# Kernel tuning notes

Hardware: AMD Instinct MI355X
Metric: run time of the kernel (lower is better)

## Reference

```python
import jax, jax.numpy as jnp
import numpy as np


def setup_inputs() -> dict:
    key = jax.random.key(0)
    ks = jax.random.split(key, 6)
    B, C1, C2, C, H, W = 16, 512, 320, 256, 64, 64
    x1 = jax.random.normal(ks[0], (B, C1, H, W), dtype=jnp.float32)
    x2 = jax.random.normal(ks[1], (B, C2, H, W), dtype=jnp.float32)
    # 1x1 conv weights, bias=False -> plain channel matmuls
    w_img = jax.random.normal(ks[2], (C, C1), dtype=jnp.float32) * (1.0 / np.sqrt(C1))
    w_txt = jax.random.normal(ks[3], (C, C2), dtype=jnp.float32) * (1.0 / np.sqrt(C2))
    w_out = jax.random.normal(ks[4], (C1, C), dtype=jnp.float32) * (1.0 / np.sqrt(C))
    gamma = jax.random.normal(ks[5], (1,), dtype=jnp.float32)
    return {"x1": x1, "x2": x2, "w_img": w_img, "w_txt": w_txt,
            "w_out": w_out, "gamma": gamma}


def reference(x1, x2, w_img, w_txt, w_out, gamma):
    B, _, H, W = x1.shape
    # 1x1 conv projections (bias-free) == channel matmuls
    img = jnp.einsum('oc,bchw->bohw', w_img, x1)   # [B,C,H,W]
    txt = jnp.einsum('oc,bchw->bohw', w_txt, x2)   # [B,C,H,W]
    C = img.shape[1]
    q = img.reshape(B, C, H * W)                    # [B,C,N]
    kv = txt.reshape(B, C, H * W)                   # [B,C,N]
    attn = jnp.einsum('bcn,bdn->bcd', q, kv)        # QK^T over spatial dim
    attn = jax.nn.softmax(attn, axis=-1)            # [B,C,C]
    attn_info = jnp.einsum('bcd,bdn->bcn', attn, kv).reshape(B, C, H, W)
    out = gamma[0] * attn_info + img                # scale-residual
    out = jnp.einsum('oc,bchw->bohw', w_out, out)   # output 1x1 conv
    return out
```

## Files before the change

### kernel.cpp

```cpp
#include <hip/hip_runtime.h>
#include <stdint.h>

typedef _Float16 f16_t;
typedef _Float16 f16x4 __attribute__((ext_vector_type(4)));
typedef _Float16 f16x8 __attribute__((ext_vector_type(8)));
typedef float f32x4 __attribute__((ext_vector_type(4)));

__device__ __forceinline__ void async16(const void* g, void* lds) {
    typedef __attribute__((address_space(3))) void lds_void;
    typedef __attribute__((address_space(1))) void glb_void;
    lds_void* l = (lds_void*)(unsigned int)(unsigned long long)lds;
    glb_void* gp = (glb_void*)(unsigned long long)g;
    __builtin_amdgcn_global_load_lds(gp, l, 16, 0, 0);
}

__global__ void cvt3_zero(const float* __restrict__ a, f16_t* __restrict__ oa, int na,
                          const float* __restrict__ b, f16_t* __restrict__ ob, int nb,
                          const float* __restrict__ c, f16_t* __restrict__ oc, int nc,
                          float4* __restrict__ z, int nz4) {
    int i = blockIdx.x * 256 + threadIdx.x;
    if (i < na) oa[i] = (f16_t)a[i];
    if (i < nb) ob[i] = (f16_t)b[i];
    if (i < nc) oc[i] = (f16_t)c[i];
    if (i < nz4) { float4 zz; zz.x = 0.f; zz.y = 0.f; zz.z = 0.f; zz.w = 0.f; z[i] = zz; }
}

template <typename TIN>
__global__ void transpose_cvt(const TIN* __restrict__ in, f16_t* __restrict__ out,
                              int R, int S, long long inStride, long long outStride) {
    __shared__ float tile[32][33];
    const int b = blockIdx.z;
    const TIN* ip = in + (long long)b * inStride;
    f16_t* op = out + (long long)b * outStride;
    const int s0 = blockIdx.x * 32;
    const int r0 = blockIdx.y * 32;
    const int t = threadIdx.x;
    const int lr = t >> 3;
    const int lc = (t & 7) * 4;

    const TIN* src = ip + (long long)(r0 + lr) * S + s0 + lc;
    float v0, v1, v2, v3;
    if (sizeof(TIN) == 4) {
        float4 v = *(const float4*)src;
        v0 = v.x; v1 = v.y; v2 = v.z; v3 = v.w;
    } else {
        f16x4 v = *(const f16x4*)src;
        v0 = (float)v[0]; v1 = (float)v[1]; v2 = (float)v[2]; v3 = (float)v[3];
    }
    tile[lr][lc + 0] = v0;
    tile[lr][lc + 1] = v1;
    tile[lr][lc + 2] = v2;
    tile[lr][lc + 3] = v3;
    __syncthreads();

    const int sr = t >> 3;
    const int rc = (t & 7) * 4;
    f16x4 o;
    o[0] = (f16_t)tile[rc + 0][sr];
    o[1] = (f16_t)tile[rc + 1][sr];
    o[2] = (f16_t)tile[rc + 2][sr];
    o[3] = (f16_t)tile[rc + 3][sr];
    *(f16x4*)(op + (long long)(s0 + sr) * R + r0 + rc) = o;
}

template <int BM, int BN, int TM, int TN, int WM, int WN, int MODE, int KSPLIT>
__global__ __launch_bounds__(256, 2)
void gemm_bt(const f16_t* __restrict__ A, const f16_t* __restrict__ B,
             void* __restrict__ C, const f16_t* __restrict__ resid,
             const float* __restrict__ gamma, f16_t* __restrict__ Ct,
             int M, int N, int K,
             long long strideA, long long strideB, long long strideC,
             long long strideCt) {
    constexpr int BK = 32;
    __shared__ __align__(16) f16_t As[BM * BK];
    __shared__ __align__(16) f16_t Bs[BN * BK];
    __shared__ __align__(16) f16_t Lt[(MODE == 3) ? BN * (BM + 8) : 1];

    const int tid = threadIdx.x;
    const int wave = tid >> 6;
    const int lane = tid & 63;
    const int wm = wave / WN;
    const int wn = wave % WN;
    const int l16 = lane & 15;
    const int l4 = lane >> 4;

    const long long zb = (KSPLIT == 1) ? blockIdx.z : (blockIdx.z / KSPLIT);
    const int ks = (KSPLIT == 1) ? 0 : (blockIdx.z % KSPLIT);
    const int Ksl = K / KSPLIT;
    const f16_t* Ab = A + zb * strideA + (long long)blockIdx.y * BM * K;
    const f16_t* Bb = B + zb * strideB + (long long)blockIdx.x * BN * K;

    f32x4 zero = {0.f, 0.f, 0.f, 0.f};
    f32x4 acc[TM][TN];
#pragma unroll
    for (int i = 0; i < TM; ++i)
#pragma unroll
        for (int j = 0; j < TN; ++j) acc[i][j] = zero;

    const int kBeg = ks * Ksl;
    for (int k0 = kBeg; k0 < kBeg + Ksl; k0 += BK) {
#pragma unroll
        for (int r = 0; r < (BM * 4) / 256; ++r) {
            int seg = r * 256 + tid;
            const f16_t* g = Ab + (long long)(seg >> 2) * K + k0 + (seg & 3) * 8;
            async16(g, &As[(r * 256 + wave * 64) * 8]);
        }
#pragma unroll
        for (int r = 0; r < (BN * 4) / 256; ++r) {
            int seg = r * 256 + tid;
            const f16_t* g = Bb + (long long)(seg >> 2) * K + k0 + (seg & 3) * 8;
            async16(g, &Bs[(r * 256 + wave * 64) * 8]);
        }
        __syncthreads();

        f16x8 af[TM], bfr[TN];
#pragma unroll
        for (int i = 0; i < TM; ++i)
            af[i] = *(const f16x8*)&As[((wm * TM + i) * 16 + l16) * BK + l4 * 8];
#pragma unroll
        for (int j = 0; j < TN; ++j)
            bfr[j] = *(const f16x8*)&Bs[((wn * TN + j) * 16 + l16) * BK + l4 * 8];
#pragma unroll
        for (int i = 0; i < TM; ++i)
#pragma unroll
            for (int j = 0; j < TN; ++j)
                acc[i][j] = __builtin_amdgcn_mfma_f32_16x16x32_f16(af[i], bfr[j], acc[i][j], 0, 0, 0);
        __syncthreads();
    }

    const int row0 = blockIdx.y * BM + wm * TM * 16;
    const int col0 = blockIdx.x * BN + wn * TN * 16;
    float g = (MODE == 2) ? gamma[0] : 0.f;
#pragma unroll
    for (int i = 0; i < TM; ++i) {
#pragma unroll
        for (int j = 0; j < TN; ++j) {
            f16x4 tq;
#pragma unroll
            for (int r = 0; r < 4; ++r) {
                int row = row0 + i * 16 + l4 * 4 + r;
                int col = col0 + j * 16 + l16;
                long long idx = zb * strideC + (long long)row * N + col;
                float v = acc[i][j][r];
                if (MODE == 0) {
                    ((f16_t*)C)[idx] = (f16_t)v;
                } else if (MODE == 1) {
                    ((float*)C)[idx] = v;
                } else if (MODE == 2) {
                    float im = (float)resid[idx];
                    ((f16_t*)C)[idx] = (f16_t)(g * v + im);
                } else if (MODE == 3) {
                    ((f16_t*)C)[idx] = (f16_t)v;
                    tq[r] = (f16_t)v;
                } else if (MODE == 5) {
                    atomicAdd(&((float*)C)[idx], v);
                }
            }
            if (MODE == 3) {
                int rl = wm * (TM * 16) + i * 16 + l4 * 4;
                int cl = wn * (TN * 16) + j * 16 + l16;
                *(f16x4*)&Lt[cl * (BM + 8) + rl] = tq;
            }
        }
    }

    if (MODE == 3) {
        __syncthreads();
        const int bx0 = blockIdx.x * BN;
        const int by0 = blockIdx.y * BM;
        const long long cb = zb * strideCt;
#pragma unroll
        for (int it = 0; it < (BM * BN) / 2048; ++it) {
            int nl = it * 16 + (tid >> 4);
            int c8 = (tid & 15) * 8;
            f16x8 v = *(const f16x8*)&Lt[nl * (BM + 8) + c8];
            *(f16x8*)&Ct[cb + (long long)(bx0 + nl) * M + by0 + c8] = v;
        }
    }
}

__global__ void softmax256(const float* __restrict__ attn, f16_t* __restrict__ out) {
    const int row = blockIdx.x * 4 + (threadIdx.x >> 6);
    const int lane = threadIdx.x & 63;
    const float4 v = *(const float4*)(attn + (long long)row * 256 + lane * 4);
    float m = fmaxf(fmaxf(v.x, v.y), fmaxf(v.z, v.w));
#pragma unroll
    for (int off = 32; off > 0; off >>= 1) m = fmaxf(m, __shfl_xor(m, off, 64));
    float e0 = __expf(v.x - m), e1 = __expf(v.y - m);
    float e2 = __expf(v.z - m), e3 = __expf(v.w - m);
    float s = e0 + e1 + e2 + e3;
#pragma unroll
    for (int off = 32; off > 0; off >>= 1) s += __shfl_xor(s, off, 64);
    const float inv = 1.0f / s;
    f16x4 o;
    o[0] = (f16_t)(e0 * inv);
    o[1] = (f16_t)(e1 * inv);
    o[2] = (f16_t)(e2 * inv);
    o[3] = (f16_t)(e3 * inv);
    *(f16x4*)(out + (long long)row * 256 + lane * 4) = o;
}

extern "C" void kernel_launch(void* const* d_in, const int* in_sizes, int n_in,
                              void* d_out, int out_size, void* d_ws, size_t ws_size,
                              hipStream_t stream) {
    (void)in_sizes; (void)n_in; (void)out_size; (void)ws_size;

    const float* x1 = (const float*)d_in[0];
    const float* x2 = (const float*)d_in[1];
    const float* w_img = (const float*)d_in[2];
    const float* w_txt = (const float*)d_in[3];
    const float* w_out = (const float*)d_in[4];
    const float* gamma = (const float*)d_in[5];

    constexpr int B = 16, C1 = 512, C2 = 320, C = 256, N = 4096, OC = 512;
    constexpr long long NC = (long long)N * C;
    constexpr long long CC = (long long)C * C;

    char* ws = (char*)d_ws;
    f16_t* wib  = (f16_t*)(ws + 0);
    f16_t* wtb  = (f16_t*)(ws + 262144);
    f16_t* wob  = (f16_t*)(ws + 425984);
    f16_t* img  = (f16_t*)(ws + 688128);
    f16_t* imgT = (f16_t*)(ws + 34242560);
    f16_t* kvT  = (f16_t*)(ws + 67796992);
    f16_t* yT   = img;

    char* oc = (char*)d_out;
    f16_t* x1t   = (f16_t*)(oc);
    f16_t* x2t   = (f16_t*)(oc + 67108864);
    f16_t* kv    = (f16_t*)(oc);
    float* attn  = (float*)(oc + 109051904);
    f16_t* attns = (f16_t*)(oc + 113246208);

    cvt3_zero<<<1024, 256, 0, stream>>>(w_img, wib, C * C1,
                                        w_txt, wtb, C * C2,
                                        w_out, wob, OC * C,
                                        (float4*)attn, (int)(B * CC / 4));

    transpose_cvt<float><<<dim3(N / 32, C1 / 32, B), 256, 0, stream>>>(
        x1, x1t, C1, N, (long long)C1 * N, (long long)N * C1);
    transpose_cvt<float><<<dim3(N / 32, C2 / 32, B), 256, 0, stream>>>(
        x2, x2t, C2, N, (long long)C2 * N, (long long)N * C2);

    gemm_bt<128, 128, 4, 4, 2, 2, 3, 1><<<dim3(N / 128, C / 128, B), 256, 0, stream>>>(
        wib, x1t, img, nullptr, nullptr, imgT, C, N, C1,
        0LL, (long long)N * C1, NC, NC);

    gemm_bt<128, 128, 4, 4, 2, 2, 3, 1><<<dim3(C / 128, N / 128, B), 256, 0, stream>>>(
        x2t, wtb, kvT, nullptr, nullptr, kv, N, C, C2,
        (long long)N * C2, 0LL, NC, NC);

    gemm_bt<64, 64, 2, 2, 2, 2, 5, 4><<<dim3(C / 64, C / 64, B * 4), 256, 0, stream>>>(
        img, kv, attn, nullptr, nullptr, nullptr, C, C, N,
        NC, NC, CC, 0LL);

    softmax256<<<(B * C) / 4, 256, 0, stream>>>(attn, attns);

    gemm_bt<128, 128, 4, 4, 2, 2, 2, 1><<<dim3(C / 128, N / 128, B), 256, 0, stream>>>(
        kvT, attns, yT, imgT, gamma, nullptr, N, C, C,
        NC, CC, NC, 0LL);

    gemm_bt<128, 128, 4, 4, 2, 2, 1, 1><<<dim3(N / 128, OC / 128, B), 256, 0, stream>>>(
        wob, yT, (float*)d_out, nullptr, nullptr, nullptr, OC, N, C,
        0LL, NC, (long long)OC * N, 0LL);
}
```

Before: 473.6 us.

## Double-buffer GEMM loads, merge prep kernels, replace atomic split-K with partial-sum reduction

After: 452.5 us. 1.05x faster.

```diff
diff --git a/kernel.cpp b/kernel.cpp
--- a/kernel.cpp
+++ b/kernel.cpp
@@ -14,53 +14,49 @@
     __builtin_amdgcn_global_load_lds(gp, l, 16, 0, 0);
 }
 
-__global__ void cvt3_zero(const float* __restrict__ a, f16_t* __restrict__ oa, int na,
-                          const float* __restrict__ b, f16_t* __restrict__ ob, int nb,
-                          const float* __restrict__ c, f16_t* __restrict__ oc, int nc,
-                          float4* __restrict__ z, int nz4) {
-    int i = blockIdx.x * 256 + threadIdx.x;
-    if (i < na) oa[i] = (f16_t)a[i];
-    if (i < nb) ob[i] = (f16_t)b[i];
-    if (i < nc) oc[i] = (f16_t)c[i];
-    if (i < nz4) { float4 zz; zz.x = 0.f; zz.y = 0.f; zz.z = 0.f; zz.w = 0.f; z[i] = zz; }
-}
-
-template <typename TIN>
-__global__ void transpose_cvt(const TIN* __restrict__ in, f16_t* __restrict__ out,
-                              int R, int S, long long inStride, long long outStride) {
+__global__ __launch_bounds__(256) void prep(
+    const float* __restrict__ x1, const float* __restrict__ x2,
+    f16_t* __restrict__ x1t, f16_t* __restrict__ x2t,
+    const float* __restrict__ w_img, f16_t* __restrict__ wib,
+    const float* __restrict__ w_txt, f16_t* __restrict__ wtb,
+    const float* __restrict__ w_out, f16_t* __restrict__ wob) {
     __shared__ float tile[32][33];
-    const int b = blockIdx.z;
-    const TIN* ip = in + (long long)b * inStride;
-    f16_t* op = out + (long long)b * outStride;
-    const int s0 = blockIdx.x * 32;
-    const int r0 = blockIdx.y * 32;
+    const int id = blockIdx.x;
     const int t = threadIdx.x;
-    const int lr = t >> 3;
-    const int lc = (t & 7) * 4;
-
-    const TIN* src = ip + (long long)(r0 + lr) * S + s0 + lc;
-    float v0, v1, v2, v3;
-    if (sizeof(TIN) == 4) {
-        float4 v = *(const float4*)src;
-        v0 = v.x; v1 = v.y; v2 = v.z; v3 = v.w;
+    if (id < 53248) {
+        const float* ip; f16_t* op; int R, bx, by, bz;
+        const int S = 4096;
+        if (id < 32768) {
+            R = 512; bx = id & 127; by = (id >> 7) & 15; bz = id >> 11;
+            ip = x1 + (long long)bz * R * S;
+            op = x1t + (long long)bz * S * R;
+        } else {
+            const int id2 = id - 32768;
+            R = 320; bx = id2 & 127; by = (id2 >> 7) % 10; bz = id2 / 1280;
+            ip = x2 + (long long)bz * R * S;
+            op = x2t + (long long)bz * S * R;
+        }
+        const int s0 = bx * 32, r0 = by * 32;
+        const int lr = t >> 3, lc = (t & 7) * 4;
+        const float4 v = *(const float4*)(ip + (long long)(r0 + lr) * S + s0 + lc);
+        tile[lr][lc + 0] = v.x;
+        tile[lr][lc + 1] = v.y;
+        tile[lr][lc + 2] = v.z;
+        tile[lr][lc + 3] = v.w;
+        __syncthreads();
+        const int sr = t >> 3, rc = (t & 7) * 4;
+        f16x4 o;
+        o[0] = (f16_t)tile[rc + 0][sr];
+        o[1] = (f16_t)tile[rc + 1][sr];
+        o[2] = (f16_t)tile[rc + 2][sr];
+        o[3] = (f16_t)tile[rc + 3][sr];
+        *(f16x4*)(op + (long long)(s0 + sr) * R + r0 + rc) = o;
     } else {
-        f16x4 v = *(const f16x4*)src;
-        v0 = (float)v[0]; v1 = (float)v[1]; v2 = (float)v[2]; v3 = (float)v[3];
-    }
-    tile[lr][lc + 0] = v0;
-    tile[lr][lc + 1] = v1;
-    tile[lr][lc + 2] = v2;
-    tile[lr][lc + 3] = v3;
-    __syncthreads();
-
-    const int sr = t >> 3;
-    const int rc = (t & 7) * 4;
-    f16x4 o;
-    o[0] = (f16_t)tile[rc + 0][sr];
-    o[1] = (f16_t)tile[rc + 1][sr];
-    o[2] = (f16_t)tile[rc + 2][sr];
-    o[3] = (f16_t)tile[rc + 3][sr];
-    *(f16x4*)(op + (long long)(s0 + sr) * R + r0 + rc) = o;
+        const int i = (id - 53248) * 256 + t;
+        if (i < 512 * 256) wib[i] = (f16_t)w_img[i];
+        if (i < 320 * 256) wtb[i] = (f16_t)w_txt[i];
+        if (i < 512 * 256) wob[i] = (f16_t)w_out[i];
+    }
 }
 
 template <int BM, int BN, int TM, int TN, int WM, int WN, int MODE, int KSPLIT>
@@ -72,9 +68,12 @@
              long long strideA, long long strideB, long long strideC,
              long long strideCt) {
     constexpr int BK = 32;
-    __shared__ __align__(16) f16_t As[BM * BK];
-    __shared__ __align__(16) f16_t Bs[BN * BK];
-    __shared__ __align__(16) f16_t Lt[(MODE == 3) ? BN * (BM + 8) : 1];
+    constexpr int AS = BM * BK;
+    constexpr int BS = BN * BK;
+    constexpr int STG = AS + BS;
+    constexpr int LT = (MODE == 3) ? BN * (BM + 8) : 0;
+    constexpr int POOL = (2 * STG > LT) ? 2 * STG : LT;
+    __shared__ __align__(16) f16_t pool[POOL];
 
     const int tid = threadIdx.x;
     const int wave = tid >> 6;
@@ -97,8 +96,9 @@
 #pragma unroll
         for (int j = 0; j < TN; ++j) acc[i][j] = zero;
 
-    const int kBeg = ks * Ksl;
-    for (int k0 = kBeg; k0 < kBeg + Ksl; k0 += BK) {
+    auto stage = [&](int b, int k0) {
+        f16_t* As = pool + b * STG;
+        f16_t* Bs = As + AS;
 #pragma unroll
         for (int r = 0; r < (BM * 4) / 256; ++r) {
             int seg = r * 256 + tid;
@@ -111,8 +111,10 @@
             const f16_t* g = Bb + (long long)(seg >> 2) * K + k0 + (seg & 3) * 8;
             async16(g, &Bs[(r * 256 + wave * 64) * 8]);
         }
-        __syncthreads();
-
+    };
+    auto compute = [&](int b) {
+        const f16_t* As = pool + b * STG;
+        const f16_t* Bs = As + AS;
         f16x8 af[TM], bfr[TN];
 #pragma unroll
         for (int i = 0; i < TM; ++i)
@@ -125,8 +127,22 @@
 #pragma unroll
             for (int j = 0; j < TN; ++j)
                 acc[i][j] = __builtin_amdgcn_mfma_f32_16x16x32_f16(af[i], bfr[j], acc[i][j], 0, 0, 0);
+    };
+
+    const int kBeg = ks * Ksl;
+    const int NT = Ksl / BK;
+    stage(0, kBeg);
+    __syncthreads();
+    int cur = 0;
+    for (int t = 1; t < NT; ++t) {
+        stage(cur ^ 1, kBeg + t * BK);
+        compute(cur);
         __syncthreads();
-    }
+        cur ^= 1;
+    }
+    compute(cur);
+
+    if (MODE == 3) __syncthreads();
 
     const int row0 = blockIdx.y * BM + wm * TM * 16;
     const int col0 = blockIdx.x * BN + wn * TN * 16;
@@ -140,26 +156,29 @@
             for (int r = 0; r < 4; ++r) {
                 int row = row0 + i * 16 + l4 * 4 + r;
                 int col = col0 + j * 16 + l16;
-                long long idx = zb * strideC + (long long)row * N + col;
                 float v = acc[i][j][r];
-                if (MODE == 0) {
-                    ((f16_t*)C)[idx] = (f16_t)v;
-                } else if (MODE == 1) {
+                if (MODE == 4) {
+                    long long idx = (long long)blockIdx.z * strideC + (long long)row * N + col;
                     ((float*)C)[idx] = v;
-                } else if (MODE == 2) {
-                    float im = (float)resid[idx];
-                    ((f16_t*)C)[idx] = (f16_t)(g * v + im);
-                } else if (MODE == 3) {
-                    ((f16_t*)C)[idx] = (f16_t)v;
-                    tq[r] = (f16_t)v;
-                } else if (MODE == 5) {
-                    atomicAdd(&((float*)C)[idx], v);
+                } else {
+                    long long idx = zb * strideC + (long long)row * N + col;
+                    if (MODE == 0) {
+                        ((f16_t*)C)[idx] = (f16_t)v;
+                    } else if (MODE == 1) {
+                        ((float*)C)[idx] = v;
+                    } else if (MODE == 2) {
+                        float im = (float)resid[idx];
+                        ((f16_t*)C)[idx] = (f16_t)(g * v + im);
+                    } else if (MODE == 3) {
+                        ((f16_t*)C)[idx] = (f16_t)v;
+                        tq[r] = (f16_t)v;
+                    }
                 }
             }
             if (MODE == 3) {
                 int rl = wm * (TM * 16) + i * 16 + l4 * 4;
                 int cl = wn * (TN * 16) + j * 16 + l16;
-                *(f16x4*)&Lt[cl * (BM + 8) + rl] = tq;
+                *(f16x4*)&pool[cl * (BM + 8) + rl] = tq;
             }
         }
     }
@@ -169,20 +188,30 @@
         const int bx0 = blockIdx.x * BN;
         const int by0 = blockIdx.y * BM;
         const long long cb = zb * strideCt;
-#pragma unroll
-        for (int it = 0; it < (BM * BN) / 2048; ++it) {
-            int nl = it * 16 + (tid >> 4);
-            int c8 = (tid & 15) * 8;
-            f16x8 v = *(const f16x8*)&Lt[nl * (BM + 8) + c8];
+        constexpr int TPR = BM / 8;
+        constexpr int RPI = 256 / TPR;
+#pragma unroll
+        for (int it = 0; it < BN / RPI; ++it) {
+            int nl = it * RPI + (tid / TPR);
+            int c8 = (tid % TPR) * 8;
+            f16x8 v = *(const f16x8*)&pool[nl * (BM + 8) + c8];
             *(f16x8*)&Ct[cb + (long long)(bx0 + nl) * M + by0 + c8] = v;
         }
     }
 }
 
-__global__ void softmax256(const float* __restrict__ attn, f16_t* __restrict__ out) {
+template <int KS>
+__global__ void softmax_red(const float* __restrict__ part, f16_t* __restrict__ out) {
     const int row = blockIdx.x * 4 + (threadIdx.x >> 6);
     const int lane = threadIdx.x & 63;
-    const float4 v = *(const float4*)(attn + (long long)row * 256 + lane * 4);
+    const int b = row >> 8, r = row & 255;
+    const float* p = part + (long long)(b * KS) * 65536 + r * 256 + lane * 4;
+    float4 v = *(const float4*)p;
+#pragma unroll
+    for (int k = 1; k < KS; ++k) {
+        float4 u = *(const float4*)(p + (long long)k * 65536);
+        v.x += u.x; v.y += u.y; v.z += u.z; v.w += u.w;
+    }
     float m = fmaxf(fmaxf(v.x, v.y), fmaxf(v.z, v.w));
 #pragma unroll
     for (int off = 32; off > 0; off >>= 1) m = fmaxf(m, __shfl_xor(m, off, 64));
@@ -197,7 +226,7 @@
     o[1] = (f16_t)(e1 * inv);
     o[2] = (f16_t)(e2 * inv);
     o[3] = (f16_t)(e3 * inv);
-    *(f16x4*)(out + (long long)row * 256 + lane * 4) = o;
+    *(f16x4*)(out + ((long long)row) * 256 + lane * 4) = o;
 }
 
 extern "C" void kernel_launch(void* const* d_in, const int* in_sizes, int n_in,
@@ -213,54 +242,47 @@
     const float* gamma = (const float*)d_in[5];
 
     constexpr int B = 16, C1 = 512, C2 = 320, C = 256, N = 4096, OC = 512;
+    constexpr int KS = 8;
     constexpr long long NC = (long long)N * C;
     constexpr long long CC = (long long)C * C;
 
     char* ws = (char*)d_ws;
-    f16_t* wib  = (f16_t*)(ws + 0);
-    f16_t* wtb  = (f16_t*)(ws + 262144);
-    f16_t* wob  = (f16_t*)(ws + 425984);
-    f16_t* img  = (f16_t*)(ws + 688128);
-    f16_t* imgT = (f16_t*)(ws + 34242560);
-    f16_t* kvT  = (f16_t*)(ws + 67796992);
-    f16_t* yT   = img;
+    f16_t* wib   = (f16_t*)(ws + 0);
+    f16_t* wtb   = (f16_t*)(ws + 262144);
+    f16_t* wob   = (f16_t*)(ws + 425984);
+    f16_t* img   = (f16_t*)(ws + 688128);
+    f16_t* imgT  = (f16_t*)(ws + 34242560);
+    f16_t* kvT   = (f16_t*)(ws + 67796992);
+    f16_t* attns = (f16_t*)(ws + 101351424);
+    f16_t* yT    = img;
 
     char* oc = (char*)d_out;
-    f16_t* x1t   = (f16_t*)(oc);
-    f16_t* x2t   = (f16_t*)(oc + 67108864);
-    f16_t* kv    = (f16_t*)(oc);
-    float* attn  = (float*)(oc + 109051904);
-    f16_t* attns = (f16_t*)(oc + 113246208);
-
-    cvt3_zero<<<1024, 256, 0, stream>>>(w_img, wib, C * C1,
-                                        w_txt, wtb, C * C2,
-                                        w_out, wob, OC * C,
-                                        (float4*)attn, (int)(B * CC / 4));
-
-    transpose_cvt<float><<<dim3(N / 32, C1 / 32, B), 256, 0, stream>>>(
-        x1, x1t, C1, N, (long long)C1 * N, (long long)N * C1);
-    transpose_cvt<float><<<dim3(N / 32, C2 / 32, B), 256, 0, stream>>>(
-        x2, x2t, C2, N, (long long)C2 * N, (long long)N * C2);
-
-    gemm_bt<128, 128, 4, 4, 2, 2, 3, 1><<<dim3(N / 128, C / 128, B), 256, 0, stream>>>(
+    f16_t* x1t  = (f16_t*)(oc);
+    f16_t* x2t  = (f16_t*)(oc + 67108864);
+    f16_t* kv   = (f16_t*)(oc);
+    float* part = (float*)(oc + 33554432);
+
+    prep<<<53760, 256, 0, stream>>>(x1, x2, x1t, x2t, w_img, wib, w_txt, wtb, w_out, wob);
+
+    gemm_bt<256, 128, 8, 4, 2, 2, 3, 1><<<dim3(N / 128, 1, B), 256, 0, stream>>>(
         wib, x1t, img, nullptr, nullptr, imgT, C, N, C1,
         0LL, (long long)N * C1, NC, NC);
 
-    gemm_bt<128, 128, 4, 4, 2, 2, 3, 1><<<dim3(C / 128, N / 128, B), 256, 0, stream>>>(
-        x2t, wtb, kvT, nullptr, nullptr, kv, N, C, C2,
-        (long long)N * C2, 0LL, NC, NC);
-
-    gemm_bt<64, 64, 2, 2, 2, 2, 5, 4><<<dim3(C / 64, C / 64, B * 4), 256, 0, stream>>>(
-        img, kv, attn, nullptr, nullptr, nullptr, C, C, N,
+    gemm_bt<256, 128, 8, 4, 2, 2, 3, 1><<<dim3(N / 128, 1, B), 256, 0, stream>>>(
+        wtb, x2t, kv, nullptr, nullptr, kvT, C, N, C2,
+        0LL, (long long)N * C2, NC, NC);
+
+    gemm_bt<64, 64, 2, 2, 2, 2, 4, KS><<<dim3(C / 64, C / 64, B * KS), 256, 0, stream>>>(
+        img, kv, part, nullptr, nullptr, nullptr, C, C, N,
         NC, NC, CC, 0LL);
 
-    softmax256<<<(B * C) / 4, 256, 0, stream>>>(attn, attns);
+    softmax_red<KS><<<(B * C) / 4, 256, 0, stream>>>(part, attns);
 
     gemm_bt<128, 128, 4, 4, 2, 2, 2, 1><<<dim3(C / 128, N / 128, B), 256, 0, stream>>>(
         kvT, attns, yT, imgT, gamma, nullptr, N, C, C,
         NC, CC, NC, 0LL);
 
-    gemm_bt<128, 128, 4, 4, 2, 2, 1, 1><<<dim3(N / 128, OC / 128, B), 256, 0, stream>>>(
+    gemm_bt<256, 128, 8, 4, 2, 2, 1, 1><<<dim3(N / 128, OC / 256, B), 256, 0, stream>>>(
         wob, yT, (float*)d_out, nullptr, nullptr, nullptr, OC, N, C,
         0LL, NC, (long long)OC * N, 0LL);
 }
```
